# Optimization experiments

Hardware: AMD Instinct MI355X
Metric: run time of the kernel (lower is better)

Reference implementation:

```python
import jax, jax.numpy as jnp
import numpy as np

N_NODES = 100000
N_EDGES = 1600000
F_IN = 128
HID = 64
N_CLASSES = 1
N_GRAPHS = 1024


def gcn_conv(x, src, dst, deg_inv_sqrt, W, b):
    # PyG GCNConv: out = D^{-1/2}(A+I)D^{-1/2} X W + b
    xw = x @ W  # [N, H]
    norm = deg_inv_sqrt[src] * deg_inv_sqrt[dst]  # [E]
    msg = xw[src] * norm[:, None]  # gather + scale
    agg = jax.ops.segment_sum(msg, dst, num_segments=N_NODES)
    # self-loop contribution: norm_ii = deg_inv_sqrt[i]^2
    agg = agg + xw * (deg_inv_sqrt ** 2)[:, None]
    return agg + b


def setup_inputs() -> dict:
    key = jax.random.key(0)
    ks = jax.random.split(key, 12)
    x = jax.random.normal(ks[0], (N_NODES, F_IN), dtype=jnp.float32)
    edge_index = jax.random.randint(ks[1], (2, N_EDGES), 0, N_NODES, dtype=jnp.int64)
    batch = jnp.sort(jax.random.randint(ks[2], (N_NODES,), 0, N_GRAPHS, dtype=jnp.int64))
    def glorot(k, fan_in, fan_out):
        s = (6.0 / (fan_in + fan_out)) ** 0.5
        return jax.random.uniform(k, (fan_in, fan_out), dtype=jnp.float32, minval=-s, maxval=s)
    W1 = glorot(ks[3], F_IN, HID); b1 = jnp.zeros((HID,), jnp.float32)
    W2 = glorot(ks[4], HID, HID); b2 = jnp.zeros((HID,), jnp.float32)
    W3 = glorot(ks[5], HID, HID); b3 = jnp.zeros((HID,), jnp.float32)
    Wl = glorot(ks[6], HID, N_CLASSES); bl = jnp.zeros((N_CLASSES,), jnp.float32)
    return {"x": x, "edge_index": edge_index, "batch": batch,
            "W1": W1, "b1": b1, "W2": W2, "b2": b2, "W3": W3, "b3": b3,
            "Wl": Wl, "bl": bl}


def reference(x, edge_index, batch, W1, b1, W2, b2, W3, b3, Wl, bl):
    src, dst = edge_index[0], edge_index[1]
    # degree with self-loops: deg[i] = (# incoming edges at i) + 1
    deg = jax.ops.segment_sum(jnp.ones((N_EDGES,), x.dtype), dst, num_segments=N_NODES) + 1.0
    deg_inv_sqrt = jax.lax.rsqrt(deg)
    h = jax.nn.relu(gcn_conv(x, src, dst, deg_inv_sqrt, W1, b1))
    # dropout: identity in eval mode
    h = jax.nn.relu(gcn_conv(h, src, dst, deg_inv_sqrt, W2, b2))
    h = gcn_conv(h, src, dst, deg_inv_sqrt, W3, b3)
    # global_mean_pool over graph ids
    sums = jax.ops.segment_sum(h, batch, num_segments=N_GRAPHS)
    counts = jax.ops.segment_sum(jnp.ones((N_NODES,), h.dtype), batch, num_segments=N_GRAPHS)
    pooled = sums / jnp.maximum(counts, 1.0)[:, None]  # [G, HID]
    return pooled @ Wl + bl  # [G, num_classes]
```

## Files before the change

kernel.cpp:

```cpp
#include <hip/hip_runtime.h>
#include <hip/hip_bf16.h>

#define N_NODES 100000
#define N_EDGES 1600000
#define F_IN 128
#define HID 64
#define N_GRAPHS 1024

#define SH 9
#define NBU 196
#define NB 200
#define BCAP 9728
#define EPB 8192
#define NSLICE 2

typedef __attribute__((ext_vector_type(8))) short bf16x8;
typedef __attribute__((ext_vector_type(4))) float f32x4;
typedef __attribute__((ext_vector_type(4))) unsigned int u32x4;

__device__ __forceinline__ unsigned short f2bf(float f) {
    __hip_bfloat16 h = __float2bfloat16(f);
    return *reinterpret_cast<unsigned short*>(&h);
}
__device__ __forceinline__ float bf2f(unsigned int u) {
    return __uint_as_float(u << 16);
}

__device__ __forceinline__ float loadf(const void* p, size_t i, int f32) {
    if (f32) return ((const float*)p)[i];
    return __bfloat162float(((const __hip_bfloat16*)p)[i]);
}
__device__ __forceinline__ int loadi(const void* p, size_t i, int i64) {
    if (i64) return (int)((const long long*)p)[i];
    return ((const int*)p)[i];
}

__global__ void k_init(const unsigned int* __restrict__ xw_,
                       const unsigned int* __restrict__ ei_,
                       int* __restrict__ flags,
                       int* __restrict__ gcnt, int* __restrict__ bcnt) {
    __shared__ int cnt_f, cnt_i;
    int t = threadIdx.x;
    if (t == 0) { cnt_f = 0; cnt_i = 0; }
    __syncthreads();
    unsigned int w = xw_[t];
    unsigned int e = (w >> 7) & 0xFFu;
    if (e >= 100u && e <= 140u) atomicAdd(&cnt_f, 1);
    unsigned int iw = ei_[2 * t + 1];
    if (iw == 0u) atomicAdd(&cnt_i, 1);
    for (int i = t; i < N_GRAPHS; i += 256) gcnt[i] = 0;
    for (int i = t; i < NB; i += 256) bcnt[i] = 0;
    __syncthreads();
    if (t == 0) {
        flags[0] = (cnt_f < 180) ? 1 : 0;
        flags[1] = (cnt_i >= 128) ? 1 : 0;
    }
}

__global__ __launch_bounds__(256) void k_part(const void* __restrict__ ei,
                                              const void* __restrict__ batch,
                                              int* __restrict__ bcnt,
                                              int* __restrict__ gcnt,
                                              unsigned int* __restrict__ packed,
                                              const int* __restrict__ flags) {
    int I64 = flags[1];
    __shared__ int hist[NB];
    __shared__ int base[NB];
    __shared__ int ghist[N_GRAPHS];
    __shared__ unsigned int elds[EPB];
    __shared__ unsigned char ebkt[EPB];
    int t = threadIdx.x;
    if (t < NB) hist[t] = 0;
    for (int i = t; i < N_GRAPHS; i += 256) ghist[i] = 0;
    __syncthreads();
    for (int it = 0; it < 2; ++it) {
        int n = blockIdx.x * 512 + it * 256 + t;
        if (n < N_NODES) atomicAdd(&ghist[loadi(batch, n, I64)], 1);
    }
    int e0 = blockIdx.x * EPB;
#pragma unroll 4
    for (int it = 0; it < EPB / 256; ++it) {
        int idx = it * 256 + t;
        int e = e0 + idx;
        unsigned int pv = 0u;
        unsigned char bk = 0xFFu;
        if (e < N_EDGES) {
            int sN = loadi(ei, e, I64);
            int d = loadi(ei, (size_t)N_EDGES + e, I64);
            bk = (unsigned char)(d >> SH);
            pv = ((unsigned int)sN << SH) | (unsigned int)(d & 511);
            atomicAdd(&hist[d >> SH], 1);
        }
        elds[idx] = pv;
        ebkt[idx] = bk;
    }
    __syncthreads();
    if (t < NB) {
        base[t] = hist[t] ? atomicAdd(&bcnt[t], hist[t]) : 0;
        hist[t] = 0;
    }
    for (int i = t; i < N_GRAPHS; i += 256)
        if (ghist[i]) atomicAdd(&gcnt[i], ghist[i]);
    __syncthreads();
#pragma unroll 4
    for (int it = 0; it < EPB / 256; ++it) {
        int idx = it * 256 + t;
        unsigned char bk = ebkt[idx];
        if (bk != 0xFFu) {
            unsigned int pv = elds[idx];
            int r = atomicAdd(&hist[bk], 1);
            int pos = base[bk] + r;
            if (pos < BCAP)
                packed[(size_t)bk * BCAP + pos] = pv;
        }
    }
}

__global__ __launch_bounds__(256) void k_hist(const unsigned int* __restrict__ packed,
                                              const int* __restrict__ bcnt,
                                              int* __restrict__ cnt,
                                              float* __restrict__ dis,
                                              int* __restrict__ partN) {
    __shared__ int hist[512];
    int b = blockIdx.x;
    int t = threadIdx.x;
    int n = bcnt[b];
    if (n > BCAP) n = BCAP;
    for (int i = t; i < 512; i += 256) hist[i] = 0;
    __syncthreads();
    const unsigned int* pb = packed + (size_t)b * BCAP;
    for (int i = t; i < n; i += 256)
        atomicAdd(&hist[pb[i] & 511u], 1);
    __syncthreads();
    int nbase = b << SH;
    for (int i = t; i < 512; i += 256) {
        int node = nbase + i;
        if (node < N_NODES) {
            int c = hist[i];
            cnt[node] = c;
            dis[node] = rsqrtf((float)c + 1.0f);
        }
    }
    __syncthreads();
    for (int off = 128; off > 0; off >>= 1) {
        if (t < off) { hist[t] += hist[t + off]; hist[256 + t] += hist[256 + t + off]; }
        __syncthreads();
    }
    if (t == 0) {
        partN[2 * b] = hist[0];
        if (2 * b + 1 < 391) partN[2 * b + 1] = hist[256];
    }
}

__global__ void k_scan_mid(int* __restrict__ partial, int nb,
                           int* __restrict__ rp, int n,
                           const int* __restrict__ gcnt, int* __restrict__ gptr) {
    __shared__ int s[512];
    int t = threadIdx.x;
    int v = (t < nb) ? partial[t] : 0;
    s[t] = v;
    __syncthreads();
    for (int off = 1; off < 512; off <<= 1) {
        int x = (t >= off) ? s[t - off] : 0;
        __syncthreads();
        s[t] += x;
        __syncthreads();
    }
    if (t < nb) partial[t] = s[t] - v;
    if (t == 511) rp[n] = s[511];
    __syncthreads();
    int a = gcnt[2 * t], bq = gcnt[2 * t + 1];
    int ps = a + bq;
    s[t] = ps;
    __syncthreads();
    for (int off = 1; off < 512; off <<= 1) {
        int x = (t >= off) ? s[t - off] : 0;
        __syncthreads();
        s[t] += x;
        __syncthreads();
    }
    int excl = s[t] - ps;
    gptr[2 * t] = excl;
    gptr[2 * t + 1] = excl + a;
    if (t == 511) gptr[1024] = s[511];
}

__global__ void k_scan_p3(const int* __restrict__ in, const int* __restrict__ partial,
                          int* __restrict__ out, int n) {
    __shared__ int s[256];
    int t = threadIdx.x;
    int i = blockIdx.x * 256 + t;
    int v = (i < n) ? in[i] : 0;
    s[t] = v;
    __syncthreads();
    for (int off = 1; off < 256; off <<= 1) {
        int x = (t >= off) ? s[t - off] : 0;
        __syncthreads();
        s[t] += x;
        __syncthreads();
    }
    if (i < n) out[i] = partial[blockIdx.x] + s[t] - v;
}

__global__ __launch_bounds__(512) void k_bucketcsr(const unsigned int* __restrict__ packed,
                                                   const int* __restrict__ bcnt,
                                                   const int* __restrict__ rp,
                                                   int* __restrict__ csr) {
    __shared__ int offs[512];
    __shared__ int elds[BCAP];
    int b = blockIdx.x;
    int nbase = b << SH;
    int base = rp[nbase];
    int lim = nbase + 512; if (lim > N_NODES) lim = N_NODES;
    int nedge = rp[lim] - base;
    if (nedge > BCAP) nedge = BCAP;
    for (int i = threadIdx.x; i < 512; i += 512) {
        int node = nbase + i;
        offs[i] = (node < N_NODES) ? (rp[node] - base) : nedge;
    }
    __syncthreads();
    int n = bcnt[b]; if (n > BCAP) n = BCAP;
    const unsigned int* pb = packed + (size_t)b * BCAP;
    for (int i = threadIdx.x; i < n; i += 512) {
        unsigned int p = pb[i];
        int pos = atomicAdd(&offs[p & 511u], 1);
        if (pos < BCAP) elds[pos] = (int)(p >> SH);
    }
    __syncthreads();
    for (int i = threadIdx.x; i < nedge; i += 512)
        csr[base + i] = elds[i];
}

template <int K>
__global__ __launch_bounds__(256) void k_gemm(const void* __restrict__ x,
                                              const void* __restrict__ W,
                                              const float* __restrict__ dis,
                                              unsigned short* __restrict__ out,
                                              const int* __restrict__ flags,
                                              int x_is_f32, int in_sm) {
    int Wf32 = flags[0];
    int xF32 = (x_is_f32 < 0) ? Wf32 : x_is_f32;
    __shared__ unsigned short Wt[64][K + 8];
    __shared__ unsigned short xs[32][K + 8];
    int t = threadIdx.x;
    int wave = t >> 6, lane = t & 63;
    int quad = lane >> 4, l16 = lane & 15;

    for (int id = t; id < 64 * K; id += 256) {
        int k = id >> 6, n = id & 63;
        Wt[n][k] = f2bf(loadf(W, id, Wf32));
    }
    __syncthreads();

    bf16x8 bfrag[K / 32];
#pragma unroll
    for (int c = 0; c < K / 32; ++c)
        bfrag[c] = *reinterpret_cast<bf16x8*>(&Wt[wave * 16 + l16][c * 32 + quad * 8]);

    const int ngroups = (N_NODES + 31) / 32;
    for (int g = blockIdx.x; g < ngroups; g += gridDim.x) {
        __syncthreads();
        int row0 = g * 32;
        if (in_sm) {
            for (int cid = t; cid < 4 * K; cid += 256) {
                int slice = cid >> 7, i = cid & 127;
                int rr = i >> 2, qq = i & 3;
                int r = row0 + rr;
                u32x4 val = {0u, 0u, 0u, 0u};
                if (r < N_NODES)
                    val = ((const u32x4*)x)[((size_t)slice * N_NODES + row0) * 4 + i];
                *reinterpret_cast<u32x4*>(&xs[rr][slice * 32 + qq * 8]) = val;
            }
        } else {
            for (int cid = t; cid < 4 * K; cid += 256) {
                int rr = cid / (K / 8), c8 = cid % (K / 8);
                int r = row0 + rr;
                u32x4 val = {0u, 0u, 0u, 0u};
                if (r < N_NODES) {
                    size_t base = (size_t)r * K + c8 * 8;
                    if (xF32) {
                        const u32x4* xp = (const u32x4*)x;
                        u32x4 q0 = xp[base / 4];
                        u32x4 q1 = xp[base / 4 + 1];
                        val.x = f2bf(__uint_as_float(q0.x)) | ((unsigned int)f2bf(__uint_as_float(q0.y)) << 16);
                        val.y = f2bf(__uint_as_float(q0.z)) | ((unsigned int)f2bf(__uint_as_float(q0.w)) << 16);
                        val.z = f2bf(__uint_as_float(q1.x)) | ((unsigned int)f2bf(__uint_as_float(q1.y)) << 16);
                        val.w = f2bf(__uint_as_float(q1.z)) | ((unsigned int)f2bf(__uint_as_float(q1.w)) << 16);
                    } else {
                        val = ((const u32x4*)x)[base / 8];
                    }
                }
                *reinterpret_cast<u32x4*>(&xs[rr][c8 * 8]) = val;
            }
        }
        __syncthreads();

        f32x4 acc0 = {0.f, 0.f, 0.f, 0.f};
        f32x4 acc1 = {0.f, 0.f, 0.f, 0.f};
#pragma unroll
        for (int c = 0; c < K / 32; ++c) {
            bf16x8 a0 = *reinterpret_cast<bf16x8*>(&xs[l16][c * 32 + quad * 8]);
            bf16x8 a1 = *reinterpret_cast<bf16x8*>(&xs[16 + l16][c * 32 + quad * 8]);
            acc0 = __builtin_amdgcn_mfma_f32_16x16x32_bf16(a0, bfrag[c], acc0, 0, 0, 0);
            acc1 = __builtin_amdgcn_mfma_f32_16x16x32_bf16(a1, bfrag[c], acc1, 0, 0, 0);
        }
        int col = wave * 16 + l16;
        unsigned short* ow = out + (size_t)(col >> 5) * (N_NODES * 32);
        int f = col & 31;
#pragma unroll
        for (int reg = 0; reg < 4; ++reg) {
            int r0 = row0 + quad * 4 + reg;
            if (r0 < N_NODES) ow[(size_t)r0 * 32 + f] = f2bf(acc0[reg] * dis[r0]);
            int r1 = row0 + 16 + quad * 4 + reg;
            if (r1 < N_NODES) ow[(size_t)r1 * 32 + f] = f2bf(acc1[reg] * dis[r1]);
        }
    }
}

__global__ __launch_bounds__(256) void k_gather_sm(const int* __restrict__ rp,
                                                   const int* __restrict__ csr,
                                                   const float* __restrict__ dis,
                                                   const unsigned short* __restrict__ xws,
                                                   const void* __restrict__ bias,
                                                   unsigned short* __restrict__ out,
                                                   int do_relu,
                                                   const int* __restrict__ flags) {
    int F32 = flags[0];
    int blk = blockIdx.x;
    int xcd = blk & 7;
    int s = xcd >> 2;
    int grp = ((blk >> 3) << 2) | (xcd & 3);
    int wave = threadIdx.x >> 6, lane = threadIdx.x & 63;
    int nodesub = lane >> 4;
    int eslot = (lane >> 2) & 3;
    int q = lane & 3;
    const u32x4* xs4 = (const u32x4*)(xws + (size_t)s * N_NODES * 32);
    u32x4* op = (u32x4*)out + (size_t)s * N_NODES * 4;
    float bb0 = loadf(bias, s * 32 + q * 8 + 0, F32);
    float bb1 = loadf(bias, s * 32 + q * 8 + 1, F32);
    float bb2 = loadf(bias, s * 32 + q * 8 + 2, F32);
    float bb3 = loadf(bias, s * 32 + q * 8 + 3, F32);
    float bb4 = loadf(bias, s * 32 + q * 8 + 4, F32);
    float bb5 = loadf(bias, s * 32 + q * 8 + 5, F32);
    float bb6 = loadf(bias, s * 32 + q * 8 + 6, F32);
    float bb7 = loadf(bias, s * 32 + q * 8 + 7, F32);
    int wbase = grp * 64 + wave * 16;

    for (int ni = 0; ni < 4; ++ni) {
        int node = wbase + ni * 4 + nodesub;
        int valid = node < N_NODES;
        int start = valid ? rp[node] : 0;
        int end = valid ? rp[node + 1] : 0;
        float a0 = 0.f, a1 = 0.f, a2 = 0.f, a3 = 0.f;
        float a4 = 0.f, a5 = 0.f, a6 = 0.f, a7 = 0.f;
        int j = start + eslot;
        if (j < end) {
            int src = csr[j];
            for (;;) {
                int jn = j + 4;
                int sn = (jn < end) ? csr[jn] : 0;
                u32x4 v = xs4[(size_t)src * 4 + q];
                a0 += bf2f(v.x & 0xFFFFu); a1 += bf2f(v.x >> 16);
                a2 += bf2f(v.y & 0xFFFFu); a3 += bf2f(v.y >> 16);
                a4 += bf2f(v.z & 0xFFFFu); a5 += bf2f(v.z >> 16);
                a6 += bf2f(v.w & 0xFFFFu); a7 += bf2f(v.w >> 16);
                if (jn >= end) break;
                j = jn; src = sn;
            }
        }
#pragma unroll
        for (int off = 4; off <= 8; off <<= 1) {
            a0 += __shfl_down(a0, off, 64); a1 += __shfl_down(a1, off, 64);
            a2 += __shfl_down(a2, off, 64); a3 += __shfl_down(a3, off, 64);
            a4 += __shfl_down(a4, off, 64); a5 += __shfl_down(a5, off, 64);
            a6 += __shfl_down(a6, off, 64); a7 += __shfl_down(a7, off, 64);
        }
        if (((lane & 12) == 0) && valid) {
            u32x4 sv = xs4[(size_t)node * 4 + q];
            float dn = dis[node];
            float v0 = fmaf(a0 + bf2f(sv.x & 0xFFFFu), dn, bb0);
            float v1 = fmaf(a1 + bf2f(sv.x >> 16),     dn, bb1);
            float v2 = fmaf(a2 + bf2f(sv.y & 0xFFFFu), dn, bb2);
            float v3 = fmaf(a3 + bf2f(sv.y >> 16),     dn, bb3);
            float v4 = fmaf(a4 + bf2f(sv.z & 0xFFFFu), dn, bb4);
            float v5 = fmaf(a5 + bf2f(sv.z >> 16),     dn, bb5);
            float v6 = fmaf(a6 + bf2f(sv.w & 0xFFFFu), dn, bb6);
            float v7 = fmaf(a7 + bf2f(sv.w >> 16),     dn, bb7);
            if (do_relu) {
                v0 = fmaxf(v0, 0.f); v1 = fmaxf(v1, 0.f); v2 = fmaxf(v2, 0.f); v3 = fmaxf(v3, 0.f);
                v4 = fmaxf(v4, 0.f); v5 = fmaxf(v5, 0.f); v6 = fmaxf(v6, 0.f); v7 = fmaxf(v7, 0.f);
            }
            u32x4 o;
            o.x = (unsigned int)f2bf(v0) | ((unsigned int)f2bf(v1) << 16);
            o.y = (unsigned int)f2bf(v2) | ((unsigned int)f2bf(v3) << 16);
            o.z = (unsigned int)f2bf(v4) | ((unsigned int)f2bf(v5) << 16);
            o.w = (unsigned int)f2bf(v6) | ((unsigned int)f2bf(v7) << 16);
            op[(size_t)node * 4 + q] = o;
        }
    }
}

__global__ __launch_bounds__(256) void k_pool_final(const int* __restrict__ gptr,
                             const unsigned short* __restrict__ h,
                             const void* __restrict__ Wl, const void* __restrict__ bl,
                             void* __restrict__ out, const int* __restrict__ flags) {
    int F32 = flags[0];
    __shared__ float part[4];
    int g = blockIdx.x;
    int w = threadIdx.x >> 6;
    int s = w >> 1;
    int wo = w & 1;
    int lane = threadIdx.x & 63;
    int nsub = lane >> 4, up = lane & 15;
    int s0 = gptr[g], e0 = gptr[g + 1];
    const unsigned int* xsl = (const unsigned int*)h + (size_t)s * N_NODES * 16;
    float a0 = 0.f, a1 = 0.f;
    for (int n = s0 + wo * 4 + nsub; n < e0; n += 8) {
        unsigned int v = xsl[(size_t)n * 16 + up];
        a0 += bf2f(v & 0xFFFFu);
        a1 += bf2f(v >> 16);
    }
    a0 += __shfl_down(a0, 32, 64); a1 += __shfl_down(a1, 32, 64);
    a0 += __shfl_down(a0, 16, 64); a1 += __shfl_down(a1, 16, 64);
    float v = 0.f;
    if (nsub == 0) {
        float cnt = fmaxf((float)(e0 - s0), 1.0f);
        int f = s * 32 + up * 2;
        v = (a0 / cnt) * loadf(Wl, f, F32) + (a1 / cnt) * loadf(Wl, f + 1, F32);
    }
    v += __shfl_down(v, 8, 64);
    v += __shfl_down(v, 4, 64);
    v += __shfl_down(v, 2, 64);
    v += __shfl_down(v, 1, 64);
    if (lane == 0) part[w] = v;
    __syncthreads();
    if (threadIdx.x == 0) {
        float r = part[0] + part[1] + part[2] + part[3] + loadf(bl, 0, F32);
        if (F32) ((float*)out)[g] = r;
        else     ((__hip_bfloat16*)out)[g] = __float2bfloat16(r);
    }
}

extern "C" void kernel_launch(void* const* d_in, const int* in_sizes, int n_in,
                              void* d_out, int out_size, void* d_ws, size_t ws_size,
                              hipStream_t stream) {
    const void* x     = d_in[0];
    const void* ei    = d_in[1];
    const void* batch = d_in[2];
    const void* W1 = d_in[3];
    const void* b1 = d_in[4];
    const void* W2 = d_in[5];
    const void* b2 = d_in[6];
    const void* W3 = d_in[7];
    const void* b3 = d_in[8];
    const void* Wl = d_in[9];
    const void* bl = d_in[10];

    float* dis   = (float*)d_ws;
    int*   cnt   = (int*)(dis + 100352);
    int*   rp    = cnt + 100352;
    int*   csr   = rp + 100352;
    int*   gcnt  = csr + 1600000;
    int*   gptr  = gcnt + 1024;
    int*   partN = gptr + 1056;
    int*   bcnt  = partN + 512;
    int*   flags = bcnt + 256;
    unsigned int* packed = (unsigned int*)(flags + 16);
    unsigned short* bufA = (unsigned short*)(packed + (size_t)NB * BCAP);
    unsigned short* bufB = bufA + (size_t)NSLICE * N_NODES * 32;

    const int TB = 256;
    dim3 blk(TB);
    int gN = (N_NODES + TB - 1) / TB;
    int gGA = 391 * 8;

    k_init<<<1, blk, 0, stream>>>((const unsigned int*)x, (const unsigned int*)ei,
                                  flags, gcnt, bcnt);
    k_part<<<(N_EDGES + EPB - 1) / EPB, blk, 0, stream>>>(ei, batch, bcnt, gcnt, packed, flags);
    k_hist<<<NBU, blk, 0, stream>>>(packed, bcnt, cnt, dis, partN);
    k_scan_mid<<<1, 512, 0, stream>>>(partN, gN, rp, N_NODES, gcnt, gptr);
    k_scan_p3<<<gN, blk, 0, stream>>>(cnt, partN, rp, N_NODES);
    k_bucketcsr<<<NBU, 512, 0, stream>>>(packed, bcnt, rp, csr);

    k_gemm<F_IN><<<1024, blk, 0, stream>>>(x, W1, dis, bufA, flags, -1, 0);
    k_gather_sm<<<gGA, blk, 0, stream>>>(rp, csr, dis, bufA, b1, bufB, 1, flags);
    k_gemm<HID><<<1024, blk, 0, stream>>>(bufB, W2, dis, bufA, flags, 0, 1);
    k_gather_sm<<<gGA, blk, 0, stream>>>(rp, csr, dis, bufA, b2, bufB, 1, flags);
    k_gemm<HID><<<1024, blk, 0, stream>>>(bufB, W3, dis, bufA, flags, 0, 1);
    k_gather_sm<<<gGA, blk, 0, stream>>>(rp, csr, dis, bufA, b3, bufB, 0, flags);

    k_pool_final<<<N_GRAPHS, blk, 0, stream>>>(gptr, bufB, Wl, bl, d_out, flags);
}
```

Before: 345.8 us.

## Fuse degree histogram, scan and CSR build into one per-bucket kernel

Replaces the histogram, two-level global scan and bucket-CSR kernels with a single per-bucket kernel. It computes local degrees, does an in-block scan, and writes CSR at fixed bucket offsets (b*BCAP), with per-node (start,end) pairs stored as int2. This removes three launches and the global prefix-sum dependency at the cost of a padded CSR layout. Edges per partition block also drop from 8192 to 2048, so k_part launches more blocks for more parallelism but does more global bucket-count atomics.

```diff
diff --git a/kernel.cpp b/kernel.cpp
--- a/kernel.cpp
+++ b/kernel.cpp
@@ -11,7 +11,7 @@
 #define NBU 196
 #define NB 200
 #define BCAP 9728
-#define EPB 8192
+#define EPB 2048
 #define NSLICE 2
 
 typedef __attribute__((ext_vector_type(8))) short bf16x8;
@@ -73,8 +73,8 @@
     if (t < NB) hist[t] = 0;
     for (int i = t; i < N_GRAPHS; i += 256) ghist[i] = 0;
     __syncthreads();
-    for (int it = 0; it < 2; ++it) {
-        int n = blockIdx.x * 512 + it * 256 + t;
+    if (t < 128) {
+        int n = blockIdx.x * 128 + t;
         if (n < N_NODES) atomicAdd(&ghist[loadi(batch, n, I64)], 1);
     }
     int e0 = blockIdx.x * EPB;
@@ -116,59 +116,55 @@
     }
 }
 
-__global__ __launch_bounds__(256) void k_hist(const unsigned int* __restrict__ packed,
-                                              const int* __restrict__ bcnt,
-                                              int* __restrict__ cnt,
-                                              float* __restrict__ dis,
-                                              int* __restrict__ partN) {
+__global__ __launch_bounds__(512) void k_csr(const unsigned int* __restrict__ packed,
+                                             const int* __restrict__ bcnt,
+                                             float* __restrict__ dis,
+                                             int2* __restrict__ rp2,
+                                             int* __restrict__ csr) {
     __shared__ int hist[512];
+    __shared__ int offs[512];
+    __shared__ int elds[BCAP];
     int b = blockIdx.x;
     int t = threadIdx.x;
-    int n = bcnt[b];
-    if (n > BCAP) n = BCAP;
-    for (int i = t; i < 512; i += 256) hist[i] = 0;
+    int n = bcnt[b]; if (n > BCAP) n = BCAP;
+    hist[t] = 0;
     __syncthreads();
     const unsigned int* pb = packed + (size_t)b * BCAP;
-    for (int i = t; i < n; i += 256)
+    for (int i = t; i < n; i += 512)
         atomicAdd(&hist[pb[i] & 511u], 1);
     __syncthreads();
-    int nbase = b << SH;
-    for (int i = t; i < 512; i += 256) {
-        int node = nbase + i;
-        if (node < N_NODES) {
-            int c = hist[i];
-            cnt[node] = c;
-            dis[node] = rsqrtf((float)c + 1.0f);
-        }
-    }
-    __syncthreads();
-    for (int off = 128; off > 0; off >>= 1) {
-        if (t < off) { hist[t] += hist[t + off]; hist[256 + t] += hist[256 + t + off]; }
-        __syncthreads();
-    }
-    if (t == 0) {
-        partN[2 * b] = hist[0];
-        if (2 * b + 1 < 391) partN[2 * b + 1] = hist[256];
-    }
-}
-
-__global__ void k_scan_mid(int* __restrict__ partial, int nb,
-                           int* __restrict__ rp, int n,
-                           const int* __restrict__ gcnt, int* __restrict__ gptr) {
+    int c = hist[t];
+    offs[t] = c;
+    __syncthreads();
+    for (int off = 1; off < 512; off <<= 1) {
+        int x = (t >= off) ? offs[t - off] : 0;
+        __syncthreads();
+        offs[t] += x;
+        __syncthreads();
+    }
+    int excl = offs[t] - c;
+    int node = (b << SH) + t;
+    int base = b * BCAP;
+    if (node < N_NODES) {
+        dis[node] = rsqrtf((float)c + 1.0f);
+        rp2[node] = make_int2(base + excl, base + excl + c);
+    }
+    __syncthreads();
+    offs[t] = excl;
+    __syncthreads();
+    for (int i = t; i < n; i += 512) {
+        unsigned int p = pb[i];
+        int pos = atomicAdd(&offs[p & 511u], 1);
+        if (pos < BCAP) elds[pos] = (int)(p >> SH);
+    }
+    __syncthreads();
+    for (int i = t; i < n; i += 512)
+        csr[base + i] = elds[i];
+}
+
+__global__ void k_gscan(const int* __restrict__ gcnt, int* __restrict__ gptr) {
     __shared__ int s[512];
     int t = threadIdx.x;
-    int v = (t < nb) ? partial[t] : 0;
-    s[t] = v;
-    __syncthreads();
-    for (int off = 1; off < 512; off <<= 1) {
-        int x = (t >= off) ? s[t - off] : 0;
-        __syncthreads();
-        s[t] += x;
-        __syncthreads();
-    }
-    if (t < nb) partial[t] = s[t] - v;
-    if (t == 511) rp[n] = s[511];
-    __syncthreads();
     int a = gcnt[2 * t], bq = gcnt[2 * t + 1];
     int ps = a + bq;
     s[t] = ps;
@@ -183,52 +179,6 @@
     gptr[2 * t] = excl;
     gptr[2 * t + 1] = excl + a;
     if (t == 511) gptr[1024] = s[511];
-}
-
-__global__ void k_scan_p3(const int* __restrict__ in, const int* __restrict__ partial,
-                          int* __restrict__ out, int n) {
-    __shared__ int s[256];
-    int t = threadIdx.x;
-    int i = blockIdx.x * 256 + t;
-    int v = (i < n) ? in[i] : 0;
-    s[t] = v;
-    __syncthreads();
-    for (int off = 1; off < 256; off <<= 1) {
-        int x = (t >= off) ? s[t - off] : 0;
-        __syncthreads();
-        s[t] += x;
-        __syncthreads();
-    }
-    if (i < n) out[i] = partial[blockIdx.x] + s[t] - v;
-}
-
-__global__ __launch_bounds__(512) void k_bucketcsr(const unsigned int* __restrict__ packed,
-                                                   const int* __restrict__ bcnt,
-                                                   const int* __restrict__ rp,
-                                                   int* __restrict__ csr) {
-    __shared__ int offs[512];
-    __shared__ int elds[BCAP];
-    int b = blockIdx.x;
-    int nbase = b << SH;
-    int base = rp[nbase];
-    int lim = nbase + 512; if (lim > N_NODES) lim = N_NODES;
-    int nedge = rp[lim] - base;
-    if (nedge > BCAP) nedge = BCAP;
-    for (int i = threadIdx.x; i < 512; i += 512) {
-        int node = nbase + i;
-        offs[i] = (node < N_NODES) ? (rp[node] - base) : nedge;
-    }
-    __syncthreads();
-    int n = bcnt[b]; if (n > BCAP) n = BCAP;
-    const unsigned int* pb = packed + (size_t)b * BCAP;
-    for (int i = threadIdx.x; i < n; i += 512) {
-        unsigned int p = pb[i];
-        int pos = atomicAdd(&offs[p & 511u], 1);
-        if (pos < BCAP) elds[pos] = (int)(p >> SH);
-    }
-    __syncthreads();
-    for (int i = threadIdx.x; i < nedge; i += 512)
-        csr[base + i] = elds[i];
 }
 
 template <int K>
@@ -317,7 +267,7 @@
     }
 }
 
-__global__ __launch_bounds__(256) void k_gather_sm(const int* __restrict__ rp,
+__global__ __launch_bounds__(256) void k_gather_sm(const int2* __restrict__ rp2,
                                                    const int* __restrict__ csr,
                                                    const float* __restrict__ dis,
                                                    const unsigned short* __restrict__ xws,
@@ -349,8 +299,8 @@
     for (int ni = 0; ni < 4; ++ni) {
         int node = wbase + ni * 4 + nodesub;
         int valid = node < N_NODES;
-        int start = valid ? rp[node] : 0;
-        int end = valid ? rp[node + 1] : 0;
+        int2 se = valid ? rp2[node] : make_int2(0, 0);
+        int start = se.x, end = se.y;
         float a0 = 0.f, a1 = 0.f, a2 = 0.f, a3 = 0.f;
         float a4 = 0.f, a5 = 0.f, a6 = 0.f, a7 = 0.f;
         int j = start + eslot;
@@ -457,13 +407,11 @@
     const void* bl = d_in[10];
 
     float* dis   = (float*)d_ws;
-    int*   cnt   = (int*)(dis + 100352);
-    int*   rp    = cnt + 100352;
-    int*   csr   = rp + 100352;
-    int*   gcnt  = csr + 1600000;
+    int2*  rp2   = (int2*)(dis + 100352);
+    int*   csr   = (int*)(rp2 + 100352);
+    int*   gcnt  = csr + NB * BCAP;
     int*   gptr  = gcnt + 1024;
-    int*   partN = gptr + 1056;
-    int*   bcnt  = partN + 512;
+    int*   bcnt  = gptr + 1056;
     int*   flags = bcnt + 256;
     unsigned int* packed = (unsigned int*)(flags + 16);
     unsigned short* bufA = (unsigned short*)(packed + (size_t)NB * BCAP);
@@ -471,23 +419,20 @@
 
     const int TB = 256;
     dim3 blk(TB);
-    int gN = (N_NODES + TB - 1) / TB;
     int gGA = 391 * 8;
 
     k_init<<<1, blk, 0, stream>>>((const unsigned int*)x, (const unsigned int*)ei,
                                   flags, gcnt, bcnt);
     k_part<<<(N_EDGES + EPB - 1) / EPB, blk, 0, stream>>>(ei, batch, bcnt, gcnt, packed, flags);
-    k_hist<<<NBU, blk, 0, stream>>>(packed, bcnt, cnt, dis, partN);
-    k_scan_mid<<<1, 512, 0, stream>>>(partN, gN, rp, N_NODES, gcnt, gptr);
-    k_scan_p3<<<gN, blk, 0, stream>>>(cnt, partN, rp, N_NODES);
-    k_bucketcsr<<<NBU, 512, 0, stream>>>(packed, bcnt, rp, csr);
+    k_csr<<<NBU, 512, 0, stream>>>(packed, bcnt, dis, rp2, csr);
+    k_gscan<<<1, 512, 0, stream>>>(gcnt, gptr);
 
     k_gemm<F_IN><<<1024, blk, 0, stream>>>(x, W1, dis, bufA, flags, -1, 0);
-    k_gather_sm<<<gGA, blk, 0, stream>>>(rp, csr, dis, bufA, b1, bufB, 1, flags);
+    k_gather_sm<<<gGA, blk, 0, stream>>>(rp2, csr, dis, bufA, b1, bufB, 1, flags);
     k_gemm<HID><<<1024, blk, 0, stream>>>(bufB, W2, dis, bufA, flags, 0, 1);
-    k_gather_sm<<<gGA, blk, 0, stream>>>(rp, csr, dis, bufA, b2, bufB, 1, flags);
+    k_gather_sm<<<gGA, blk, 0, stream>>>(rp2, csr, dis, bufA, b2, bufB, 1, flags);
     k_gemm<HID><<<1024, blk, 0, stream>>>(bufB, W3, dis, bufA, flags, 0, 1);
-    k_gather_sm<<<gGA, blk, 0, stream>>>(rp, csr, dis, bufA, b3, bufB, 0, flags);
+    k_gather_sm<<<gGA, blk, 0, stream>>>(rp2, csr, dis, bufA, b3, bufB, 0, flags);
 
     k_pool_final<<<N_GRAPHS, blk, 0, stream>>>(gptr, bufB, Wl, bl, d_out, flags);
 }
```

Result: faster. 338.5 us (-2.1%).
